# Kernel tuning notes

Measured on AMD Instinct MI355X. Metric: run time of the kernel, lower is better.

Reference implementation:

```python
import jax, jax.numpy as jnp
import numpy as np

N_NODES = 100000
N_EDGES = 1600000
F_IN = 512
D_EMB = 128
D_HID = 64
N_CLS = 32
EPS = 1e-5


def setup_inputs() -> dict:
    key = jax.random.key(0)
    ks = jax.random.split(key, 16)
    def w(k, shape):
        fan_in = shape[0]
        return jax.random.normal(k, shape, dtype=jnp.float32) / jnp.sqrt(jnp.float32(fan_in))
    return {
        "x": jax.random.normal(ks[0], (N_NODES, F_IN), dtype=jnp.float32),
        "W1": w(ks[1], (F_IN, D_EMB)), "b1": jnp.zeros((D_EMB,), jnp.float32),
        "Wc1": w(ks[2], (D_EMB, D_HID)), "bc1": jnp.zeros((D_HID,), jnp.float32),
        "Wc2": w(ks[3], (D_HID, D_HID)), "bc2": jnp.zeros((D_HID,), jnp.float32),
        "Wc3": w(ks[4], (D_HID, D_HID)), "bc3": jnp.zeros((D_HID,), jnp.float32),
        "gamma": jnp.ones((D_HID,), jnp.float32), "beta": jnp.zeros((D_HID,), jnp.float32),
        "W2": w(ks[5], (D_HID, N_CLS)), "b2": jnp.zeros((N_CLS,), jnp.float32),
        "W3": w(ks[6], (N_CLS, N_CLS)), "b3": jnp.zeros((N_CLS,), jnp.float32),
        "edge_index": jax.random.randint(ks[7], (2, N_EDGES), 0, N_NODES, dtype=jnp.int32),
    }


def _agg_mean(h, src, dst, n):
    # gather source-node features along edges, sum into destination nodes, divide by degree
    s = jax.ops.segment_sum(h[src], dst, num_segments=n)          # [N, d]
    deg = jax.ops.segment_sum(jnp.ones((src.shape[0], 1), h.dtype), dst, num_segments=n)
    return s / jnp.maximum(deg, 1.0)


def _conv1p(h, src, dst, W, b):
    # ConvolutionalLayer_1P: neighborhood gather/aggregate -> linear -> relu
    return jax.nn.relu(_agg_mean(h, src, dst, h.shape[0]) @ W + b)


def reference(x, W1, b1, Wc1, bc1, Wc2, bc2, Wc3, bc3, gamma, beta, W2, b2, W3, b3, edge_index):
    src, dst = edge_index[0], edge_index[1]
    # linmaps1 on 0th-order ptensors == identity copy
    h = jax.nn.relu(x @ W1 + b1)                 # lin1 + relu (dropout = identity in eval)
    h = _conv1p(h, src, dst, Wc1, bc1)           # conv1
    h = _conv1p(h, src, dst, Wc2, bc2)           # conv2
    h = _conv1p(h, src, dst, Wc3, bc3)           # conv3
    mean = jnp.mean(h, axis=0)
    var = jnp.var(h, axis=0)
    h = (h - mean) * jax.lax.rsqrt(var + EPS) * gamma + beta  # batchnorm (batch stats)
    h = jax.nn.relu(h @ W2 + b2)                 # lin2 + relu (dropout = identity)
    out = h @ W3 + b3                            # lin3; linmaps0 == identity
    return out
```

## Files before the change

kernel.cpp:

```cpp
#include <hip/hip_runtime.h>
#include <cstdint>
#include <cstddef>

constexpr int F_IN  = 512;
constexpr int D_EMB = 128;
constexpr int D_HID = 64;
constexpr int N_CLS = 32;

typedef __attribute__((ext_vector_type(8))) short short8;
typedef __attribute__((ext_vector_type(4))) float floatx4;

__device__ inline unsigned short f2bf(float f) {
  union { float f; uint32_t u; } v; v.f = f;
  uint32_t r = v.u + 0x7FFF + ((v.u >> 16) & 1);
  return (unsigned short)(r >> 16);
}

__global__ __launch_bounds__(256) void wt_kernel(
    const float* __restrict__ W1, short8* __restrict__ Wt2)
{
  int idx = blockIdx.x * 256 + threadIdx.x;
  int kc8 = idx >> 10, lin = idx & 1023;
  int ct = lin >> 7, rem = lin & 127, ks = rem >> 6, ln = rem & 63;
  int col = ct * 16 + (ln & 15);
  int k0 = kc8 * 64 + ks * 32 + (ln >> 4) * 8;
  short8 s;
#pragma unroll
  for (int j = 0; j < 8; ++j)
    s[j] = (short)f2bf(W1[(size_t)(k0 + j) * D_EMB + col]);
  Wt2[idx] = s;
}

__global__ __launch_bounds__(256) void lin1_mfma_kernel(
    const float* __restrict__ X, const short8* __restrict__ Wt2,
    const float* __restrict__ b1, float* __restrict__ H1, int n)
{
  __shared__ short8 Ws[1024];
  __shared__ short8 Xs[1024];

  const int t = threadIdx.x;
  const int wave = t >> 6, lane = t & 63;
  const int quad = lane >> 4, mrow = lane & 15;
  const int node0 = blockIdx.x * 128;
  const int rloc = (wave >> 1) * 64;
  const int cw = (wave & 1) * 4;

  const float* sp[4];
  int soff[4];
#pragma unroll
  for (int i = 0; i < 4; ++i) {
    int g = t + i * 256;
    int row = g >> 3, col8 = g & 7;
    soff[i] = row * 128 + ((col8 * 16) ^ ((row & 7) << 4));
    int gr = node0 + row; if (gr >= n) gr = n - 1;
    sp[i] = &X[(size_t)gr * F_IN + col8 * 8];
  }

  floatx4 acc[4][4];
#pragma unroll
  for (int i = 0; i < 4; ++i)
#pragma unroll
    for (int j = 0; j < 4; ++j) acc[i][j] = (floatx4){0.f, 0.f, 0.f, 0.f};

  float4 xr[4][2];
  short8 wr[4];

#pragma unroll
  for (int i = 0; i < 4; ++i) {
    const float* p = sp[i];
    xr[i][0] = *(const float4*)p;
    xr[i][1] = *(const float4*)(p + 4);
    wr[i] = Wt2[t + i * 256];
  }

  for (int kc8 = 0; kc8 < 8; ++kc8) {
    short8 s8[4];
#pragma unroll
    for (int i = 0; i < 4; ++i) {
      s8[i][0] = (short)f2bf(xr[i][0].x); s8[i][1] = (short)f2bf(xr[i][0].y);
      s8[i][2] = (short)f2bf(xr[i][0].z); s8[i][3] = (short)f2bf(xr[i][0].w);
      s8[i][4] = (short)f2bf(xr[i][1].x); s8[i][5] = (short)f2bf(xr[i][1].y);
      s8[i][6] = (short)f2bf(xr[i][1].z); s8[i][7] = (short)f2bf(xr[i][1].w);
    }
    __syncthreads();
#pragma unroll
    for (int i = 0; i < 4; ++i) {
      *(short8*)((char*)Xs + soff[i]) = s8[i];
      Ws[t + i * 256] = wr[i];
    }
    __syncthreads();

    if (kc8 < 7) {
#pragma unroll
      for (int i = 0; i < 4; ++i) {
        const float* p = sp[i] + (kc8 + 1) * 64;
        xr[i][0] = *(const float4*)p;
        xr[i][1] = *(const float4*)(p + 4);
        wr[i] = Wt2[(kc8 + 1) * 1024 + t + i * 256];
      }
    }

#pragma unroll
    for (int ks = 0; ks < 2; ++ks) {
      short8 af[4], bf[4];
#pragma unroll
      for (int rt = 0; rt < 4; ++rt) {
        int row = rloc + rt * 16 + mrow;
        int byteoff = row * 128 + ((ks * 64 + quad * 16) ^ ((row & 7) << 4));
        af[rt] = *(const short8*)((const char*)Xs + byteoff);
      }
#pragma unroll
      for (int c = 0; c < 4; ++c)
        bf[c] = Ws[((cw + c) * 2 + ks) * 64 + lane];
#pragma unroll
      for (int rt = 0; rt < 4; ++rt)
#pragma unroll
        for (int c = 0; c < 4; ++c)
          acc[rt][c] = __builtin_amdgcn_mfma_f32_16x16x32_bf16(
              af[rt], bf[c], acc[rt][c], 0, 0, 0);
    }
  }

  const int rowbase = node0 + rloc;
#pragma unroll
  for (int ct = 0; ct < 4; ++ct) {
    int col = (cw + ct) * 16 + mrow;
    float bias = b1[col];
#pragma unroll
    for (int rt = 0; rt < 4; ++rt) {
#pragma unroll
      for (int r = 0; r < 4; ++r) {
        int gn = rowbase + rt * 16 + quad * 4 + r;
        if (gn < n)
          H1[(size_t)gn * D_EMB + col] = fmaxf(acc[rt][ct][r] + bias, 0.f);
      }
    }
  }
}

template<int K>
__global__ __launch_bounds__(256) void mm_kernel(
    const float* __restrict__ In, const float* __restrict__ W,
    float* __restrict__ Out, int n)
{
  __shared__ float Hs[64][K + 4];
  __shared__ float Ws[K][64];
  const int t = threadIdx.x;
  const int node0 = blockIdx.x * 64;
  constexpr int KQ = K / 4;

#pragma unroll
  for (int i = 0; i < (64 * KQ) / 256; ++i) {
    int lin = t + i * 256;
    int node = lin / KQ, kq = lin % KQ;
    int gn = node0 + node;
    float4 v = make_float4(0.f, 0.f, 0.f, 0.f);
    if (gn < n)
      v = *(const float4*)&In[(size_t)gn * K + kq * 4];
    *(float4*)&Hs[node][kq * 4] = v;
  }
#pragma unroll
  for (int i = 0; i < (K * 64) / 1024; ++i) {
    int lin = t + i * 256;
    ((float4*)&Ws[0][0])[lin] = ((const float4*)W)[lin];
  }
  __syncthreads();

  const int rg = t >> 4, cg = t & 15;
  float acc[4][4];
#pragma unroll
  for (int i = 0; i < 4; ++i)
#pragma unroll
    for (int j = 0; j < 4; ++j) acc[i][j] = 0.f;

#pragma unroll 8
  for (int k = 0; k < K; ++k) {
    float a[4] = {Hs[rg*4+0][k], Hs[rg*4+1][k], Hs[rg*4+2][k], Hs[rg*4+3][k]};
    float4 b = *(const float4*)&Ws[k][cg * 4];
#pragma unroll
    for (int i = 0; i < 4; ++i) {
      acc[i][0] += a[i]*b.x; acc[i][1] += a[i]*b.y;
      acc[i][2] += a[i]*b.z; acc[i][3] += a[i]*b.w;
    }
  }
#pragma unroll
  for (int i = 0; i < 4; ++i) {
    int gn = node0 + rg * 4 + i;
    if (gn < n) {
      float4 o = make_float4(acc[i][0], acc[i][1], acc[i][2], acc[i][3]);
      *(float4*)&Out[(size_t)gn * 64 + cg * 4] = o;
    }
  }
}

__global__ __launch_bounds__(512) void gmm_kernel(
    const float* __restrict__ P, const int* __restrict__ offs,
    const int* __restrict__ adj, const int* __restrict__ deg,
    const float* __restrict__ bin, const float* __restrict__ W,
    float* __restrict__ Out, int n)
{
  __shared__ float Hs[64][68];
  __shared__ float Ws[64][64];
  const int t = threadIdx.x;
  const int wave = t >> 6, lane = t & 63;
  const int node0 = blockIdx.x * 64;

#pragma unroll
  for (int i = 0; i < 2; ++i) {
    int lin = t + i * 512;
    ((float4*)&Ws[0][0])[lin] = ((const float4*)W)[lin];
  }
  const float bb = bin[lane];

#pragma unroll 1
  for (int nd = 0; nd < 8; ++nd) {
    int ln = wave * 8 + nd;
    int node = node0 + ln;
    float v = 0.f;
    if (node < n) {
      int beg = offs[node], end = offs[node + 1];
      float a0 = 0.f, a1 = 0.f, a2 = 0.f, a3 = 0.f;
      int j = beg;
      while (j < end) {
        int m = min(end - j, 64);
        int idx = (lane < m) ? adj[j + lane] : 0;
        int q = 0;
        for (; q + 3 < m; q += 4) {
          int s0 = __shfl(idx, q, 64),     s1 = __shfl(idx, q + 1, 64);
          int s2 = __shfl(idx, q + 2, 64), s3 = __shfl(idx, q + 3, 64);
          a0 += P[(size_t)s0 * 64 + lane];
          a1 += P[(size_t)s1 * 64 + lane];
          a2 += P[(size_t)s2 * 64 + lane];
          a3 += P[(size_t)s3 * 64 + lane];
        }
        for (; q < m; ++q) {
          int s0 = __shfl(idx, q, 64);
          a0 += P[(size_t)s0 * 64 + lane];
        }
        j += m;
      }
      float rd = 1.f / fmaxf((float)deg[node], 1.f);
      v = fmaxf(((a0 + a2) + (a1 + a3)) * rd + bb, 0.f);
    }
    Hs[ln][lane] = v;
  }
  __syncthreads();

  const int rg = t >> 4, cg = t & 15;
  float acc[2][4];
#pragma unroll
  for (int i = 0; i < 2; ++i)
#pragma unroll
    for (int j = 0; j < 4; ++j) acc[i][j] = 0.f;

#pragma unroll 8
  for (int k = 0; k < 64; ++k) {
    float a[2] = {Hs[rg * 2 + 0][k], Hs[rg * 2 + 1][k]};
    float4 b = *(const float4*)&Ws[k][cg * 4];
#pragma unroll
    for (int i = 0; i < 2; ++i) {
      acc[i][0] += a[i]*b.x; acc[i][1] += a[i]*b.y;
      acc[i][2] += a[i]*b.z; acc[i][3] += a[i]*b.w;
    }
  }
#pragma unroll
  for (int i = 0; i < 2; ++i) {
    int gn = node0 + rg * 2 + i;
    if (gn < n) {
      float4 o = make_float4(acc[i][0], acc[i][1], acc[i][2], acc[i][3]);
      *(float4*)&Out[(size_t)gn * 64 + cg * 4] = o;
    }
  }
}

__global__ __launch_bounds__(512) void gp_kernel(
    const float* __restrict__ P, const int* __restrict__ offs,
    const int* __restrict__ adj, const int* __restrict__ deg,
    const float* __restrict__ bc3, float* __restrict__ H4,
    float* __restrict__ stats, int n)
{
  const int t = threadIdx.x;
  const int wave = t >> 6, lane = t & 63;
  const int node0 = blockIdx.x * 64;
  const float bb = bc3[lane];
  float s = 0.f, s2 = 0.f;

#pragma unroll 1
  for (int nd = 0; nd < 8; ++nd) {
    int node = node0 + wave * 8 + nd;
    if (node >= n) break;
    int beg = offs[node], end = offs[node + 1];
    float a0 = 0.f, a1 = 0.f, a2 = 0.f, a3 = 0.f;
    int j = beg;
    while (j < end) {
      int m = min(end - j, 64);
      int idx = (lane < m) ? adj[j + lane] : 0;
      int q = 0;
      for (; q + 3 < m; q += 4) {
        int s0 = __shfl(idx, q, 64),     s1 = __shfl(idx, q + 1, 64);
        int s2i = __shfl(idx, q + 2, 64), s3 = __shfl(idx, q + 3, 64);
        a0 += P[(size_t)s0 * 64 + lane];
        a1 += P[(size_t)s1 * 64 + lane];
        a2 += P[(size_t)s2i * 64 + lane];
        a3 += P[(size_t)s3 * 64 + lane];
      }
      for (; q < m; ++q) {
        int s0 = __shfl(idx, q, 64);
        a0 += P[(size_t)s0 * 64 + lane];
      }
      j += m;
    }
    float rd = 1.f / fmaxf((float)deg[node], 1.f);
    float v = fmaxf(((a0 + a2) + (a1 + a3)) * rd + bb, 0.f);
    H4[(size_t)node * 64 + lane] = v;
    s += v; s2 += v * v;
  }

  __shared__ float red[2][8][64];
  red[0][wave][lane] = s; red[1][wave][lane] = s2;
  __syncthreads();
  if (t < 128) {
    int which = t >> 6, ff = t & 63;
    float a = 0.f;
#pragma unroll
    for (int w = 0; w < 8; ++w) a += red[which][w][ff];
    atomicAdd(&stats[which * 64 + ff], a);
  }
}


__global__ __launch_bounds__(256) void hist_kernel(
    const int* __restrict__ dst, int* __restrict__ G,
    float* __restrict__ stats, int nE, int B, int NB)
{
  __shared__ int h[256];
  int blk = blockIdx.x, t = threadIdx.x;
  if (blk == 0 && t < 128) stats[t] = 0.f;
  h[t] = 0;
  __syncthreads();
  int base = blk * 8192;
  int lim = min(8192, nE - base);
  for (int i = t; i < lim; i += 256)
    atomicAdd(&h[dst[base + i] >> 9], 1);
  __syncthreads();
  if (t < NB) G[t * B + blk] = h[t];
}

__global__ __launch_bounds__(256) void scan1_kernel(
    const int* __restrict__ in, int* __restrict__ out,
    int* __restrict__ bsum, int n)
{
  __shared__ int sh[256];
  int t = threadIdx.x;
  int i = blockIdx.x * 256 + t;
  int c = (i < n) ? in[i] : 0;
  sh[t] = c;
  __syncthreads();
#pragma unroll
  for (int off = 1; off < 256; off <<= 1) {
    int v = 0;
    if (t >= off) v = sh[t - off];
    __syncthreads();
    if (t >= off) sh[t] += v;
    __syncthreads();
  }
  if (i < n) out[i] = sh[t] - c;
  if (t == 255) bsum[blockIdx.x] = sh[255];
}

__global__ __launch_bounds__(256) void scan2_kernel(int* __restrict__ bsum, int nb)
{
  __shared__ int sh[256];
  __shared__ int carry;
  int t = threadIdx.x;
  if (t == 0) carry = 0;
  __syncthreads();
  for (int base = 0; base < nb; base += 256) {
    int i = base + t;
    int v = (i < nb) ? bsum[i] : 0;
    sh[t] = v;
    __syncthreads();
#pragma unroll
    for (int off = 1; off < 256; off <<= 1) {
      int u = 0;
      if (t >= off) u = sh[t - off];
      __syncthreads();
      if (t >= off) sh[t] += u;
      __syncthreads();
    }
    int c0 = carry;
    int incl = sh[t], total = sh[255];
    if (i < nb) bsum[i] = c0 + incl - v;
    __syncthreads();
    if (t == 0) carry = c0 + total;
    __syncthreads();
  }
  if (t == 0) bsum[nb] = carry;
}

__global__ __launch_bounds__(256) void scatter2_kernel(
    const int* __restrict__ src, const int* __restrict__ dst,
    const int* __restrict__ W, const int* __restrict__ bsum,
    int2* __restrict__ EP, int nE, int B, int NB)
{
  __shared__ int cur[256];
  int blk = blockIdx.x, t = threadIdx.x;
  if (t < NB) {
    int gi = t * B + blk;
    cur[t] = W[gi] + bsum[gi >> 8];
  }
  __syncthreads();
  int base = blk * 8192;
  int lim = min(8192, nE - base);
  for (int i = t; i < lim; i += 256) {
    int s = src[base + i], d = dst[base + i];
    int slot = atomicAdd(&cur[d >> 9], 1);
    EP[slot] = make_int2(s, d);
  }
}

__global__ __launch_bounds__(256) void fillc_kernel(
    const int2* __restrict__ EP, const int* __restrict__ W,
    const int* __restrict__ bsum,
    int* __restrict__ cnt, int* __restrict__ offs, int* __restrict__ adj,
    int n, int nE, int B, int NB)
{
  __shared__ int h[512];
  int b = blockIdx.x, t = threadIdx.x;
  int g0i = b * B;
  int segStart = W[g0i] + bsum[g0i >> 8];
  int segEnd = (b == NB - 1) ? nE : (W[g0i + B] + bsum[(g0i + B) >> 8]);
  int nodeBase = b << 9;

  h[t] = 0; h[t + 256] = 0;
  __syncthreads();
  for (int i = segStart + t; i < segEnd; i += 256)
    atomicAdd(&h[EP[i].y - nodeBase], 1);
  __syncthreads();
  int c0 = h[t], c1 = h[t + 256];
#pragma unroll
  for (int off = 1; off < 512; off <<= 1) {
    int a = (t >= off) ? h[t - off] : 0;
    int bb = (t + 256 >= off) ? h[t + 256 - off] : 0;
    __syncthreads();
    h[t] += a; h[t + 256] += bb;
    __syncthreads();
  }
  int e0 = h[t] - c0, e1 = h[t + 256] - c1;
  int g0 = nodeBase + t, g1 = nodeBase + t + 256;
  if (g0 < n) { cnt[g0] = c0; offs[g0] = segStart + e0; }
  if (g1 < n) { cnt[g1] = c1; offs[g1] = segStart + e1; }
  if (b == 0 && t == 0) offs[n] = nE;
  __syncthreads();
  h[t] = e0; h[t + 256] = e1;
  __syncthreads();
  for (int i = segStart + t; i < segEnd; i += 256) {
    int2 p = EP[i];
    int slot = atomicAdd(&h[p.y - nodeBase], 1);
    adj[segStart + slot] = p.x;
  }
}

__global__ __launch_bounds__(256) void fold_kernel(
    const float* __restrict__ stats, const float* __restrict__ gamma,
    const float* __restrict__ beta, const float* __restrict__ W2,
    const float* __restrict__ b2, float* __restrict__ W2f,
    float* __restrict__ b2f, int n)
{
  __shared__ float rsg[64], corr[64];
  int t = threadIdx.x;
  if (t < 64) {
    float m = stats[t] / (float)n;
    float var = stats[64 + t] / (float)n - m * m;
    float rs = rsqrtf(var + 1e-5f);
    float g = gamma[t] * rs;
    rsg[t] = g;
    corr[t] = beta[t] - m * g;
  }
  __syncthreads();
#pragma unroll
  for (int i = 0; i < 8; ++i) {
    int lin = t + i * 256;
    int k = lin >> 5;
    W2f[lin] = rsg[k] * W2[lin];
  }
  if (t < 32) {
    float a = b2[t];
    for (int k = 0; k < 64; ++k) a += corr[k] * W2[k * 32 + t];
    b2f[t] = a;
  }
}

__global__ __launch_bounds__(256) void final_kernel(
    const float* __restrict__ H4, const float* __restrict__ W2f,
    const float* __restrict__ b2f, const float* __restrict__ W3,
    const float* __restrict__ b3, float* __restrict__ Out, int n)
{
  __shared__ float Hs[64][68];
  __shared__ float W2s[64][32];
  __shared__ float W3s[32][32];
  __shared__ float Us[64][36];
  __shared__ float b2s[32], b3s[32];
  const int t = threadIdx.x;
  const int node0 = blockIdx.x * 64;

#pragma unroll
  for (int i = 0; i < 4; ++i) {
    int lin = t + i * 256;
    int node = lin >> 4, kq = lin & 15;
    float4 v = make_float4(0.f, 0.f, 0.f, 0.f);
    if (node0 + node < n)
      v = *(const float4*)&H4[(size_t)(node0 + node) * 64 + kq * 4];
    *(float4*)&Hs[node][kq * 4] = v;
  }
#pragma unroll
  for (int i = 0; i < 2; ++i) {
    int lin = t + i * 256;
    ((float4*)&W2s[0][0])[lin] = ((const float4*)W2f)[lin];
  }
  ((float4*)&W3s[0][0])[t & 255] = ((const float4*)W3)[t & 255];
  if (t < 32) { b2s[t] = b2f[t]; b3s[t] = b3[t]; }
  __syncthreads();

  const int rg = t >> 4, cg = t & 15;
  float acc[4][2] = {{0.f,0.f},{0.f,0.f},{0.f,0.f},{0.f,0.f}};
#pragma unroll 8
  for (int k = 0; k < 64; ++k) {
    float a[4] = {Hs[rg*4+0][k], Hs[rg*4+1][k], Hs[rg*4+2][k], Hs[rg*4+3][k]};
    float w0 = W2s[k][cg*2], w1 = W2s[k][cg*2+1];
#pragma unroll
    for (int i = 0; i < 4; ++i) { acc[i][0] += a[i]*w0; acc[i][1] += a[i]*w1; }
  }
#pragma unroll
  for (int i = 0; i < 4; ++i) {
    Us[rg*4+i][cg*2+0] = fmaxf(acc[i][0] + b2s[cg*2+0], 0.f);
    Us[rg*4+i][cg*2+1] = fmaxf(acc[i][1] + b2s[cg*2+1], 0.f);
  }
  __syncthreads();

  float acc2[4][2] = {{0.f,0.f},{0.f,0.f},{0.f,0.f},{0.f,0.f}};
#pragma unroll
  for (int k = 0; k < 32; ++k) {
    float a[4] = {Us[rg*4+0][k], Us[rg*4+1][k], Us[rg*4+2][k], Us[rg*4+3][k]};
    float w0 = W3s[k][cg*2], w1 = W3s[k][cg*2+1];
#pragma unroll
    for (int i = 0; i < 4; ++i) { acc2[i][0] += a[i]*w0; acc2[i][1] += a[i]*w1; }
  }
  float (*Os)[36] = (float(*)[36])Hs;
#pragma unroll
  for (int i = 0; i < 4; ++i) {
    Os[rg*4+i][cg*2+0] = acc2[i][0] + b3s[cg*2+0];
    Os[rg*4+i][cg*2+1] = acc2[i][1] + b3s[cg*2+1];
  }
  __syncthreads();
#pragma unroll
  for (int i = 0; i < 2; ++i) {
    int lin = t + i * 256;
    int node = lin >> 3, c4 = lin & 7;
    if (node0 + node < n)
      *(float4*)&Out[(size_t)(node0 + node) * 32 + c4 * 4] =
          *(float4*)&Os[node][c4 * 4];
  }
}

extern "C" void kernel_launch(void* const* d_in, const int* in_sizes, int n_in,
                              void* d_out, int out_size, void* d_ws, size_t ws_size,
                              hipStream_t stream)
{
  const float* X     = (const float*)d_in[0];
  const float* W1    = (const float*)d_in[1];
  const float* b1    = (const float*)d_in[2];
  const float* Wc1   = (const float*)d_in[3];
  const float* bc1   = (const float*)d_in[4];
  const float* Wc2   = (const float*)d_in[5];
  const float* bc2   = (const float*)d_in[6];
  const float* Wc3   = (const float*)d_in[7];
  const float* bc3   = (const float*)d_in[8];
  const float* gamma = (const float*)d_in[9];
  const float* beta  = (const float*)d_in[10];
  const float* W2    = (const float*)d_in[11];
  const float* b2    = (const float*)d_in[12];
  const float* W3    = (const float*)d_in[13];
  const float* b3    = (const float*)d_in[14];
  const int*   ei    = (const int*)d_in[15];

  const int n  = in_sizes[0] / F_IN;
  const int nE = in_sizes[15] / 2;
  const int* src  = ei;
  const int* dstv = ei + nE;

  const int NB = (n + 511) >> 9;
  const int B  = (nE + 8191) >> 13;
  const int NG = NB * B;
  const int nbG = (NG + 255) / 256;

  float* ws    = (float*)d_ws;
  float* H1    = ws;
  float* Pa    = H1 + (size_t)n * D_EMB;
  float* Pb    = Pa + (size_t)n * D_HID;
  float* stats = Pb + (size_t)n * D_HID;
  float* W2f   = stats + 128;
  float* b2f   = W2f + 2048;
  int*   cnt   = (int*)(b2f + 32);
  int*   offs  = cnt + n;
  int*   G     = offs + n + 1;
  int*   W     = G + NG;
  int*   bsum  = W + NG + 1;
  int*   adj   = bsum + nbG + 1;
  uintptr_t epAddr = ((uintptr_t)(adj + nE) + 7) & ~(uintptr_t)7;
  int2*  EP    = (int2*)epAddr;
  short8* Wt2  = (short8*)(EP + nE);
  float* H4    = H1;

  const int nb  = (n + 63) / 64;

  wt_kernel<<<32, 256, 0, stream>>>(W1, Wt2);
  lin1_mfma_kernel<<<(n + 127) / 128, 256, 0, stream>>>(X, Wt2, b1, H1, n);

  hist_kernel<<<B, 256, 0, stream>>>(dstv, G, stats, nE, B, NB);
  scan1_kernel<<<nbG, 256, 0, stream>>>(G, W, bsum, NG);
  scan2_kernel<<<1, 256, 0, stream>>>(bsum, nbG);
  scatter2_kernel<<<B, 256, 0, stream>>>(src, dstv, W, bsum, EP, nE, B, NB);
  fillc_kernel<<<NB, 256, 0, stream>>>(EP, W, bsum, cnt, offs, adj, n, nE, B, NB);

  mm_kernel<128><<<nb, 256, 0, stream>>>(H1, Wc1, Pa, n);

  gmm_kernel<<<nb, 512, 0, stream>>>(Pa, offs, adj, cnt, bc1, Wc2, Pb, n);

  gmm_kernel<<<nb, 512, 0, stream>>>(Pb, offs, adj, cnt, bc2, Wc3, Pa, n);

  gp_kernel<<<nb, 512, 0, stream>>>(Pa, offs, adj, cnt, bc3, H4, stats, n);

  fold_kernel<<<1, 256, 0, stream>>>(stats, gamma, beta, W2, b2, W2f, b2f, n);
  final_kernel<<<nb, 256, 0, stream>>>(H4, W2f, b2f, W3, b3, (float*)d_out, n);
}
```

Before: 692.4 us.

## Fuse lin1 MFMA GEMM with conv1 weight projection into one kernel

Merges the lin1 bf16 MFMA kernel and the separate 128->64 projection by Wc1 into a single kernel. The relu'd lin1 tile stays in shared memory and is multiplied by Wc1 in two K halves, so the 100k x 128 fp32 H1 intermediate is never written to or re-read from global memory. The block tile shrinks from 128 to 64 nodes, which reduces per-block MFMA reuse of W1 and raises shared memory use to about 49 KB, possibly lowering occupancy.

After: 657.8 us. 1.05x faster.

```diff
diff --git a/kernel.cpp b/kernel.cpp
--- a/kernel.cpp
+++ b/kernel.cpp
@@ -31,24 +31,31 @@
   Wt2[idx] = s;
 }
 
-__global__ __launch_bounds__(256) void lin1_mfma_kernel(
+__global__ __launch_bounds__(256) void l1c1_kernel(
     const float* __restrict__ X, const short8* __restrict__ Wt2,
-    const float* __restrict__ b1, float* __restrict__ H1, int n)
-{
-  __shared__ short8 Ws[1024];
-  __shared__ short8 Xs[1024];
+    const float* __restrict__ b1, const float* __restrict__ Wc1,
+    float* __restrict__ P, int n)
+{
+  __shared__ __align__(16) char smem[50176];
+  short8* Xs = (short8*)smem;
+  short8* Ws = (short8*)(smem + 8192);
+  float (*Hs)[132] = (float(*)[132])smem;
+  float (*Wc)[64]  = (float(*)[64])(smem + 33792);
 
   const int t = threadIdx.x;
   const int wave = t >> 6, lane = t & 63;
   const int quad = lane >> 4, mrow = lane & 15;
-  const int node0 = blockIdx.x * 128;
-  const int rloc = (wave >> 1) * 64;
-  const int cw = (wave & 1) * 4;
-
-  const float* sp[4];
-  int soff[4];
-#pragma unroll
-  for (int i = 0; i < 4; ++i) {
+  const int node0 = blockIdx.x * 64;
+  const int cw = wave * 2;
+
+  float4 wp[4];
+#pragma unroll
+  for (int i = 0; i < 4; ++i) wp[i] = ((const float4*)Wc1)[i * 256 + t];
+
+  const float* sp[2];
+  int soff[2];
+#pragma unroll
+  for (int i = 0; i < 2; ++i) {
     int g = t + i * 256;
     int row = g >> 3, col8 = g & 7;
     soff[i] = row * 128 + ((col8 * 16) ^ ((row & 7) << 4));
@@ -56,27 +63,27 @@
     sp[i] = &X[(size_t)gr * F_IN + col8 * 8];
   }
 
-  floatx4 acc[4][4];
+  floatx4 acc[4][2];
 #pragma unroll
   for (int i = 0; i < 4; ++i)
 #pragma unroll
-    for (int j = 0; j < 4; ++j) acc[i][j] = (floatx4){0.f, 0.f, 0.f, 0.f};
-
-  float4 xr[4][2];
+    for (int j = 0; j < 2; ++j) acc[i][j] = (floatx4){0.f, 0.f, 0.f, 0.f};
+
+  float4 xr[2][2];
   short8 wr[4];
 
 #pragma unroll
-  for (int i = 0; i < 4; ++i) {
-    const float* p = sp[i];
-    xr[i][0] = *(const float4*)p;
-    xr[i][1] = *(const float4*)(p + 4);
-    wr[i] = Wt2[t + i * 256];
-  }
+  for (int i = 0; i < 2; ++i) {
+    xr[i][0] = *(const float4*)sp[i];
+    xr[i][1] = *(const float4*)(sp[i] + 4);
+  }
+#pragma unroll
+  for (int i = 0; i < 4; ++i) wr[i] = Wt2[t + i * 256];
 
   for (int kc8 = 0; kc8 < 8; ++kc8) {
-    short8 s8[4];
-#pragma unroll
-    for (int i = 0; i < 4; ++i) {
+    short8 s8[2];
+#pragma unroll
+    for (int i = 0; i < 2; ++i) {
       s8[i][0] = (short)f2bf(xr[i][0].x); s8[i][1] = (short)f2bf(xr[i][0].y);
       s8[i][2] = (short)f2bf(xr[i][0].z); s8[i][3] = (short)f2bf(xr[i][0].w);
       s8[i][4] = (short)f2bf(xr[i][1].x); s8[i][5] = (short)f2bf(xr[i][1].y);
@@ -84,111 +91,106 @@
     }
     __syncthreads();
 #pragma unroll
-    for (int i = 0; i < 4; ++i) {
+    for (int i = 0; i < 2; ++i)
       *(short8*)((char*)Xs + soff[i]) = s8[i];
+#pragma unroll
+    for (int i = 0; i < 4; ++i)
       Ws[t + i * 256] = wr[i];
-    }
     __syncthreads();
 
     if (kc8 < 7) {
 #pragma unroll
-      for (int i = 0; i < 4; ++i) {
+      for (int i = 0; i < 2; ++i) {
         const float* p = sp[i] + (kc8 + 1) * 64;
         xr[i][0] = *(const float4*)p;
         xr[i][1] = *(const float4*)(p + 4);
+      }
+#pragma unroll
+      for (int i = 0; i < 4; ++i)
         wr[i] = Wt2[(kc8 + 1) * 1024 + t + i * 256];
-      }
     }
 
 #pragma unroll
     for (int ks = 0; ks < 2; ++ks) {
-      short8 af[4], bf[4];
+      short8 af[4], bf[2];
 #pragma unroll
       for (int rt = 0; rt < 4; ++rt) {
-        int row = rloc + rt * 16 + mrow;
+        int row = rt * 16 + mrow;
         int byteoff = row * 128 + ((ks * 64 + quad * 16) ^ ((row & 7) << 4));
         af[rt] = *(const short8*)((const char*)Xs + byteoff);
       }
 #pragma unroll
-      for (int c = 0; c < 4; ++c)
+      for (int c = 0; c < 2; ++c)
         bf[c] = Ws[((cw + c) * 2 + ks) * 64 + lane];
 #pragma unroll
       for (int rt = 0; rt < 4; ++rt)
 #pragma unroll
-        for (int c = 0; c < 4; ++c)
+        for (int c = 0; c < 2; ++c)
           acc[rt][c] = __builtin_amdgcn_mfma_f32_16x16x32_bf16(
               af[rt], bf[c], acc[rt][c], 0, 0, 0);
     }
   }
 
-  const int rowbase = node0 + rloc;
-#pragma unroll
-  for (int ct = 0; ct < 4; ++ct) {
+  __syncthreads();
+#pragma unroll
+  for (int ct = 0; ct < 2; ++ct) {
     int col = (cw + ct) * 16 + mrow;
-    float bias = b1[col];
-#pragma unroll
-    for (int rt = 0; rt < 4; ++rt) {
-#pragma unroll
-      for (int r = 0; r < 4; ++r) {
-        int gn = rowbase + rt * 16 + quad * 4 + r;
-        if (gn < n)
-          H1[(size_t)gn * D_EMB + col] = fmaxf(acc[rt][ct][r] + bias, 0.f);
-      }
-    }
-  }
-}
-
-template<int K>
-__global__ __launch_bounds__(256) void mm_kernel(
-    const float* __restrict__ In, const float* __restrict__ W,
-    float* __restrict__ Out, int n)
-{
-  __shared__ float Hs[64][K + 4];
-  __shared__ float Ws[K][64];
-  const int t = threadIdx.x;
-  const int node0 = blockIdx.x * 64;
-  constexpr int KQ = K / 4;
-
-#pragma unroll
-  for (int i = 0; i < (64 * KQ) / 256; ++i) {
-    int lin = t + i * 256;
-    int node = lin / KQ, kq = lin % KQ;
-    int gn = node0 + node;
-    float4 v = make_float4(0.f, 0.f, 0.f, 0.f);
-    if (gn < n)
-      v = *(const float4*)&In[(size_t)gn * K + kq * 4];
-    *(float4*)&Hs[node][kq * 4] = v;
-  }
-#pragma unroll
-  for (int i = 0; i < (K * 64) / 1024; ++i) {
-    int lin = t + i * 256;
-    ((float4*)&Ws[0][0])[lin] = ((const float4*)W)[lin];
-  }
-  __syncthreads();
+    float b = b1[col];
+#pragma unroll
+    for (int rt = 0; rt < 4; ++rt)
+#pragma unroll
+      for (int r = 0; r < 4; ++r)
+        Hs[rt * 16 + quad * 4 + r][col] = fmaxf(acc[rt][ct][r] + b, 0.f);
+  }
+#pragma unroll
+  for (int i = 0; i < 4; ++i)
+    ((float4*)&Wc[0][0])[i * 256 + t] = wp[i];
+  __syncthreads();
+
+#pragma unroll
+  for (int i = 0; i < 4; ++i)
+    wp[i] = ((const float4*)Wc1)[1024 + i * 256 + t];
 
   const int rg = t >> 4, cg = t & 15;
-  float acc[4][4];
+  float acc2[4][4];
 #pragma unroll
   for (int i = 0; i < 4; ++i)
 #pragma unroll
-    for (int j = 0; j < 4; ++j) acc[i][j] = 0.f;
+    for (int j = 0; j < 4; ++j) acc2[i][j] = 0.f;
 
 #pragma unroll 8
-  for (int k = 0; k < K; ++k) {
+  for (int k = 0; k < 64; ++k) {
     float a[4] = {Hs[rg*4+0][k], Hs[rg*4+1][k], Hs[rg*4+2][k], Hs[rg*4+3][k]};
-    float4 b = *(const float4*)&Ws[k][cg * 4];
+    float4 b = *(const float4*)&Wc[k][cg * 4];
 #pragma unroll
     for (int i = 0; i < 4; ++i) {
-      acc[i][0] += a[i]*b.x; acc[i][1] += a[i]*b.y;
-      acc[i][2] += a[i]*b.z; acc[i][3] += a[i]*b.w;
+      acc2[i][0] += a[i]*b.x; acc2[i][1] += a[i]*b.y;
+      acc2[i][2] += a[i]*b.z; acc2[i][3] += a[i]*b.w;
+    }
+  }
+  __syncthreads();
+#pragma unroll
+  for (int i = 0; i < 4; ++i)
+    ((float4*)&Wc[0][0])[i * 256 + t] = wp[i];
+  __syncthreads();
+
+#pragma unroll 8
+  for (int k = 0; k < 64; ++k) {
+    float a[4] = {Hs[rg*4+0][64+k], Hs[rg*4+1][64+k],
+                  Hs[rg*4+2][64+k], Hs[rg*4+3][64+k]};
+    float4 b = *(const float4*)&Wc[k][cg * 4];
+#pragma unroll
+    for (int i = 0; i < 4; ++i) {
+      acc2[i][0] += a[i]*b.x; acc2[i][1] += a[i]*b.y;
+      acc2[i][2] += a[i]*b.z; acc2[i][3] += a[i]*b.w;
     }
   }
 #pragma unroll
   for (int i = 0; i < 4; ++i) {
     int gn = node0 + rg * 4 + i;
     if (gn < n) {
-      float4 o = make_float4(acc[i][0], acc[i][1], acc[i][2], acc[i][3]);
-      *(float4*)&Out[(size_t)gn * 64 + cg * 4] = o;
+      float4 o = make_float4(acc2[i][0], acc2[i][1], acc2[i][2], acc2[i][3]);
+      *(float4*)&P[(size_t)gn * 64 + cg * 4] = o;
     }
   }
 }
@@ -297,7 +299,7 @@
       int idx = (lane < m) ? adj[j + lane] : 0;
       int q = 0;
       for (; q + 3 < m; q += 4) {
-        int s0 = __shfl(idx, q, 64),     s1 = __shfl(idx, q + 1, 64);
+        int s0 = __shfl(idx, q, 64),      s1 = __shfl(idx, q + 1, 64);
         int s2i = __shfl(idx, q + 2, 64), s3 = __shfl(idx, q + 3, 64);
         a0 += P[(size_t)s0 * 64 + lane];
         a1 += P[(size_t)s1 * 64 + lane];
@@ -327,7 +329,6 @@
     atomicAdd(&stats[which * 64 + ff], a);
   }
 }
-
 
 __global__ __launch_bounds__(256) void hist_kernel(
     const int* __restrict__ dst, int* __restrict__ G,
@@ -595,8 +596,7 @@
   const int nbG = (NG + 255) / 256;
 
   float* ws    = (float*)d_ws;
-  float* H1    = ws;
-  float* Pa    = H1 + (size_t)n * D_EMB;
+  float* Pa    = ws;
   float* Pb    = Pa + (size_t)n * D_HID;
   float* stats = Pb + (size_t)n * D_HID;
   float* W2f   = stats + 128;
@@ -610,12 +610,12 @@
   uintptr_t epAddr = ((uintptr_t)(adj + nE) + 7) & ~(uintptr_t)7;
   int2*  EP    = (int2*)epAddr;
   short8* Wt2  = (short8*)(EP + nE);
-  float* H4    = H1;
+  float* H4    = Pb;
 
   const int nb  = (n + 63) / 64;
 
   wt_kernel<<<32, 256, 0, stream>>>(W1, Wt2);
-  lin1_mfma_kernel<<<(n + 127) / 128, 256, 0, stream>>>(X, Wt2, b1, H1, n);
+  l1c1_kernel<<<nb, 256, 0, stream>>>(X, Wt2, b1, Wc1, Pa, n);
 
   hist_kernel<<<B, 256, 0, stream>>>(dstv, G, stats, nE, B, NB);
   scan1_kernel<<<nbG, 256, 0, stream>>>(G, W, bsum, NG);
@@ -623,8 +623,6 @@
   scatter2_kernel<<<B, 256, 0, stream>>>(src, dstv, W, bsum, EP, nE, B, NB);
   fillc_kernel<<<NB, 256, 0, stream>>>(EP, W, bsum, cnt, offs, adj, n, nE, B, NB);
 
-  mm_kernel<128><<<nb, 256, 0, stream>>>(H1, Wc1, Pa, n);
-
   gmm_kernel<<<nb, 512, 0, stream>>>(Pa, offs, adj, cnt, bc1, Wc2, Pb, n);
 
   gmm_kernel<<<nb, 512, 0, stream>>>(Pb, offs, adj, cnt, bc2, Wc3, Pa, n);
```
